# Optimization experiments

Measured on AMD Instinct MI355X. Metric: run time of the kernel, lower is better.

The kernel has to match this reference:

```python
import jax, jax.numpy as jnp
import numpy as np

BF16_MIN = -3.3895313892515355e+38  # torch.finfo(torch.bfloat16).min
B, S, D = 2, 2048, 2048
H, KVH = 32, 8
HD = D // H  # 64


def setup_inputs() -> dict:
    key = jax.random.key(0)
    ks = jax.random.split(key, 7)
    scale = 0.02
    x = jax.random.normal(ks[0], (B, S, D), dtype=jnp.float32)
    # rotary tables as in llama2.c: theta = 10000^{-2i/hd}
    inv_freq = 1.0 / (10000.0 ** (np.arange(0, HD, 2, dtype=np.float32) / HD))
    t = np.arange(S, dtype=np.float32)
    freqs = np.outer(t, inv_freq)  # (S, HD//2)
    freqs_cos = jnp.asarray(np.cos(freqs))
    freqs_sin = jnp.asarray(np.sin(freqs))
    wq = jax.random.normal(ks[1], (H * HD, D), dtype=jnp.float32) * scale
    wk = jax.random.normal(ks[2], (KVH * HD, D), dtype=jnp.float32) * scale
    wv = jax.random.normal(ks[3], (KVH * HD, D), dtype=jnp.float32) * scale
    wo = jax.random.normal(ks[4], (D, H * HD), dtype=jnp.float32) * scale
    attn_mask = jnp.ones((B, S), dtype=jnp.int32)
    return {"x": x, "freqs_cos": freqs_cos, "freqs_sin": freqs_sin,
            "wq": wq, "wk": wk, "wv": wv, "wo": wo, "attn_mask": attn_mask}


def _rope(x, cos, sin):
    # x: (b, s, h, hd) -> split into interleaved real/imag pairs
    b, s, h, hd = x.shape
    xr = x[..., 0::2]
    xi = x[..., 1::2]
    cos = cos[None, :, None, :]  # (1, s, 1, hd//2)
    sin = sin[None, :, None, :]
    out_r = xr * cos - xi * sin
    out_i = xr * sin + xi * cos
    return jnp.stack([out_r, out_i], axis=-1).reshape(b, s, h, hd)


def reference(x, freqs_cos, freqs_sin, wq, wk, wv, wo, attn_mask):
    b, s, d = x.shape
    n_rep = H // KVH
    xq = jnp.einsum('bsd,ed->bse', x, wq).reshape(b, s, H, HD)
    xk = jnp.einsum('bsd,ed->bse', x, wk).reshape(b, s, KVH, HD)
    xv = jnp.einsum('bsd,ed->bse', x, wv).reshape(b, s, KVH, HD)
    xq = _rope(xq, freqs_cos, freqs_sin)
    xk = _rope(xk, freqs_cos, freqs_sin)
    # GQA repeat_kv: (b, s, kvh, hd) -> (b, s, kvh*n_rep, hd)
    xk = jnp.repeat(xk, n_rep, axis=2)
    xv = jnp.repeat(xv, n_rep, axis=2)
    # (b, h, s, hd)
    xq = xq.transpose(0, 2, 1, 3)
    xk = xk.transpose(0, 2, 1, 3)
    xv = xv.transpose(0, 2, 1, 3)
    causal = jnp.triu(jnp.full((s, s), BF16_MIN, dtype=x.dtype), k=1)[None, None]
    pad = jnp.where(attn_mask[:, None, :] == 0, BF16_MIN, 0.0).astype(x.dtype)  # (b,1,s) -> broadcast over query
    combined = causal + pad[:, None, :, :]  # (b,1,s,s)
    scores = jnp.einsum('bhqd,bhkd->bhqk', xq, xk) / np.sqrt(HD).astype(x.dtype)
    scores = jax.nn.softmax(scores + combined, axis=-1)
    out = jnp.einsum('bhqk,bhkd->bhqd', scores, xv)
    out = out.transpose(0, 2, 1, 3).reshape(b, s, H * HD)
    return jnp.einsum('bse,de->bsd', out, wo)
```

## Files before the change

### kernel.cpp

```cpp
#include <hip/hip_runtime.h>

typedef unsigned short u16;
typedef unsigned int u32;
typedef __attribute__((ext_vector_type(8))) short bf16x8;
typedef __attribute__((ext_vector_type(4))) float f32x4;

#define S_LEN 2048
#define QKV_N 3072
#define CEXP 0.18033688011f
#define M32C 5.77078016f

__device__ __forceinline__ u16 f2bf(float f) {
  u32 u = __builtin_bit_cast(u32, f);
  u32 r = (u + 0x7FFFu + ((u >> 16) & 1u)) >> 16;
  return (u16)r;
}
__device__ __forceinline__ float b2f(u16 h) {
  u32 u = ((u32)h) << 16;
  return __builtin_bit_cast(float, u);
}
__device__ __forceinline__ u32 cvtpk(float lo, float hi) {
  u32 r;
  asm("v_cvt_pk_bf16_f32 %0, %1, %2" : "=v"(r) : "v"(lo), "v"(hi));
  return r;
}
__device__ __forceinline__ void gload16(const void* g, void* l) {
  __builtin_amdgcn_global_load_lds(
      (const __attribute__((address_space(1))) u32*)g,
      (__attribute__((address_space(3))) u32*)l, 16, 0, 0);
}

__global__ void cast_all(const float* __restrict__ x, const float* __restrict__ wq,
                         const float* __restrict__ wk, const float* __restrict__ wv,
                         const float* __restrict__ wo, u16* __restrict__ xb,
                         u16* __restrict__ wqkvb, u16* __restrict__ wob) {
  int i = blockIdx.x * 256 + threadIdx.x;
  const float* s;
  u16* d;
  int so, dofs;
  if (i < 2097152) {
    s = x; d = xb; so = i; dofs = i;
  } else if (i < 3145728) {
    s = wq; d = wqkvb; so = i - 2097152; dofs = so;
  } else if (i < 3407872) {
    s = wk; d = wqkvb; so = i - 3145728; dofs = so + 1048576;
  } else if (i < 3670016) {
    s = wv; d = wqkvb; so = i - 3407872; dofs = so + 1310720;
  } else {
    s = wo; d = wob; so = i - 3670016; dofs = so;
  }
  float4 v = ((const float4*)s)[so];
  ((uint2*)d)[dofs] = make_uint2(cvtpk(v.x, v.y), cvtpk(v.z, v.w));
}

template <int BN, int WM, int WN, int OUT_BF16>
__global__ __launch_bounds__(512, 2) void gemm_bt2(const u16* __restrict__ A,
                                                   const u16* __restrict__ B,
                                                   void* __restrict__ Cv,
                                                   int K, int ldc, int nbx) {
  constexpr int BM = 256;
  constexpr int MR = BM / WM / 16;
  constexpr int NR = BN / WN / 16;
  constexpr int MR2 = MR / 2, NR2 = NR / 2;
  constexpr int AR = BM / 64, BR = BN / 64;
  __shared__ u16 As0[BM * 64], As1[BM * 64];
  __shared__ u16 Bs0[BN * 64], Bs1[BN * 64];

  const int tid = threadIdx.x;
  const int lane = tid & 63, w = tid >> 6;
  const int wm = w / WN, wn = w % WN;
  const int g = lane >> 4, r16 = lane & 15;
  const int swz = r16 & 7;

  const int nwg = gridDim.x;
  const int q = nwg >> 3, r = nwg & 7;
  const int xcd = blockIdx.x & 7, off = blockIdx.x >> 3;
  const int wg = (xcd < r ? xcd * (q + 1) : r * (q + 1) + (xcd - r) * q) + off;
  const int m0 = (wg / nbx) * BM, n0 = (wg % nbx) * BN;

  const int rowi = tid >> 3;
  const int scol = ((tid & 7) ^ (rowi & 7)) * 8;
  const u16* Ag0 = A + (size_t)(m0 + rowi) * K + scol;
  const u16* Bg0 = B + (size_t)(n0 + rowi) * K + scol;

  f32x4 acc[MR][NR];
#pragma unroll
  for (int mi = 0; mi < MR; ++mi)
#pragma unroll
    for (int ni = 0; ni < NR; ++ni) acc[mi][ni] = f32x4{0.f, 0.f, 0.f, 0.f};

  auto stage = [&](int kb, u16* Ad, u16* Bd) {
#pragma unroll
    for (int rr = 0; rr < AR; ++rr)
      gload16(Ag0 + (size_t)rr * 64 * K + kb, Ad + rr * 4096 + tid * 8);
#pragma unroll
    for (int rr = 0; rr < BR; ++rr)
      gload16(Bg0 + (size_t)rr * 64 * K + kb, Bd + rr * 4096 + tid * 8);
  };

  auto compute = [&](const u16* Asrc, const u16* Bsrc) {
    bf16x8 ac[MR2][2], bc[NR][2];
    const u16* Aw = Asrc + (wm * MR * 16 + r16) * 64;
    const u16* Bw = Bsrc + (wn * NR * 16 + r16) * 64;
#pragma unroll
    for (int mi = 0; mi < MR2; ++mi)
#pragma unroll
      for (int kk = 0; kk < 2; ++kk)
        ac[mi][kk] = *(const bf16x8*)(Aw + mi * 1024 + ((kk * 4 + g) ^ swz) * 8);
#pragma unroll
    for (int ni = 0; ni < NR2; ++ni)
#pragma unroll
      for (int kk = 0; kk < 2; ++kk)
        bc[ni][kk] = *(const bf16x8*)(Bw + ni * 1024 + ((kk * 4 + g) ^ swz) * 8);
    __builtin_amdgcn_s_setprio(1);
#pragma unroll
    for (int mi = 0; mi < MR2; ++mi)
#pragma unroll
      for (int ni = 0; ni < NR2; ++ni)
#pragma unroll
        for (int kk = 0; kk < 2; ++kk)
          acc[mi][ni] = __builtin_amdgcn_mfma_f32_16x16x32_bf16(
              ac[mi][kk], bc[ni][kk], acc[mi][ni], 0, 0, 0);
    __builtin_amdgcn_s_setprio(0);
#pragma unroll
    for (int ni = NR2; ni < NR; ++ni)
#pragma unroll
      for (int kk = 0; kk < 2; ++kk)
        bc[ni][kk] = *(const bf16x8*)(Bw + ni * 1024 + ((kk * 4 + g) ^ swz) * 8);
    __builtin_amdgcn_s_setprio(1);
#pragma unroll
    for (int mi = 0; mi < MR2; ++mi)
#pragma unroll
      for (int ni = NR2; ni < NR; ++ni)
#pragma unroll
        for (int kk = 0; kk < 2; ++kk)
          acc[mi][ni] = __builtin_amdgcn_mfma_f32_16x16x32_bf16(
              ac[mi][kk], bc[ni][kk], acc[mi][ni], 0, 0, 0);
    __builtin_amdgcn_s_setprio(0);
#pragma unroll
    for (int mi = 0; mi < MR2; ++mi)
#pragma unroll
      for (int kk = 0; kk < 2; ++kk)
        ac[mi][kk] =
            *(const bf16x8*)(Aw + (MR2 + mi) * 1024 + ((kk * 4 + g) ^ swz) * 8);
    __builtin_amdgcn_s_setprio(1);
#pragma unroll
    for (int mi = 0; mi < MR2; ++mi)
#pragma unroll
      for (int ni = NR2; ni < NR; ++ni)
#pragma unroll
        for (int kk = 0; kk < 2; ++kk)
          acc[MR2 + mi][ni] = __builtin_amdgcn_mfma_f32_16x16x32_bf16(
              ac[mi][kk], bc[ni][kk], acc[MR2 + mi][ni], 0, 0, 0);
    __builtin_amdgcn_s_setprio(0);
    __builtin_amdgcn_s_setprio(1);
#pragma unroll
    for (int mi = 0; mi < MR2; ++mi)
#pragma unroll
      for (int ni = 0; ni < NR2; ++ni)
#pragma unroll
        for (int kk = 0; kk < 2; ++kk)
          acc[MR2 + mi][ni] = __builtin_amdgcn_mfma_f32_16x16x32_bf16(
              ac[mi][kk], bc[ni][kk], acc[MR2 + mi][ni], 0, 0, 0);
    __builtin_amdgcn_s_setprio(0);
  };

  const int NT = K >> 6;
  stage(0, As0, Bs0);
  __syncthreads();
  for (int t = 0; t < NT; t += 2) {
    if (t + 1 < NT) stage((t + 1) * 64, As1, Bs1);
    compute(As0, Bs0);
    __syncthreads();
    if (t + 2 < NT) stage((t + 2) * 64, As0, Bs0);
    compute(As1, Bs1);
    __syncthreads();
  }

#pragma unroll
  for (int mi = 0; mi < MR; ++mi)
#pragma unroll
    for (int ni = 0; ni < NR; ++ni) {
      int row = m0 + wm * MR * 16 + mi * 16 + g * 4;
      int col = n0 + wn * NR * 16 + ni * 16 + r16;
#pragma unroll
      for (int j = 0; j < 4; ++j) {
        if (OUT_BF16)
          ((u16*)Cv)[(size_t)(row + j) * ldc + col] = f2bf(acc[mi][ni][j]);
        else
          ((float*)Cv)[(size_t)(row + j) * ldc + col] = acc[mi][ni][j];
      }
    }
}

__global__ void rope_k(u16* qkv, const float* __restrict__ fc,
                       const float* __restrict__ fs) {
  const int p = blockIdx.x * 256 + threadIdx.x;
  const int row = blockIdx.y;
  const int s = row & (S_LEN - 1);
  const int i = p & 31;
  const float c = fc[s * 32 + i], sn = fs[s * 32 + i];
  u32 v = *(const u32*)&qkv[(size_t)row * QKV_N + 2 * p];
  float xr = b2f((u16)(v & 0xffffu)), xi = b2f((u16)(v >> 16));
  float orr = xr * c - xi * sn;
  float oi = xr * sn + xi * c;
  *(u32*)&qkv[(size_t)row * QKV_N + 2 * p] = cvtpk(orr, oi);
}

__global__ void vtrans_k(const u16* __restrict__ qkv, u16* __restrict__ vt) {
  int i = blockIdx.x * 256 + threadIdx.x;
  int s = i & 2047;
  int d = (i >> 11) & 63;
  int bk = i >> 17;
  int b = bk >> 3, kv = bk & 7;
  vt[i] = qkv[(size_t)(b * 2048 + s) * QKV_N + 2560 + kv * 64 + d];
}

__global__ __launch_bounds__(256, 3) void attn_fwd(const u16* __restrict__ qkv,
                                                   const u16* __restrict__ vt,
                                                   u16* __restrict__ aout) {
  __shared__ u16 Ks[2][64 * 64];
  __shared__ u16 Vs[2][64 * 64];
  __shared__ u16 Ps[4][16 * 64];

  const int bh = blockIdx.x;
  const int y = blockIdx.y;
  const int qt = (y < 4) ? (15 - y) : (y < 8) ? (y - 4) : (y < 12) ? y : (19 - y);
  const int b = bh >> 5, h = bh & 31, kvh = h >> 2;
  const int tid = threadIdx.x;
  const int w = tid >> 6, lane = tid & 63;
  const int g = lane >> 4, r16 = lane & 15;
  const int q0w = qt * 128 + w * 32;

  const u16* kbase = qkv + (size_t)b * S_LEN * QKV_N + 2048 + kvh * 64;
  const u16* vbase = vt + (size_t)(b * 8 + kvh) * 64 * S_LEN;

  const int srow = lane >> 3;
  const int scol = ((lane & 7) * 8) ^ (srow * 8);
  const int swz = (r16 & 7) * 8;

  bf16x8 qf[2][2];
#pragma unroll
  for (int qs = 0; qs < 2; ++qs) {
    const u16* qrow =
        qkv + (size_t)(b * S_LEN + q0w + qs * 16 + r16) * QKV_N + h * 64;
#pragma unroll
    for (int dh = 0; dh < 2; ++dh)
      qf[qs][dh] = *(const bf16x8*)(qrow + dh * 32 + g * 8);
  }

  f32x4 oacc[2][4];
#pragma unroll
  for (int qs = 0; qs < 2; ++qs)
#pragma unroll
    for (int dt = 0; dt < 4; ++dt) oacc[qs][dt] = f32x4{0.f, 0.f, 0.f, 0.f};
  float lsum[2] = {0.f, 0.f};

  const int nt = qt * 2 + 2;
  const int ntw = ((q0w + 31) >> 6) + 1;

#pragma unroll
  for (int c2 = 0; c2 < 2; ++c2) {
    int c = w * 2 + c2;
    gload16(kbase + (size_t)(c * 8 + srow) * QKV_N + scol, &Ks[0][c * 512]);
    gload16(vbase + (size_t)(c * 8 + srow) * 2048 + scol, &Vs[0][c * 512]);
  }
  __syncthreads();

  int cur = 0;
  for (int t = 0; t < nt; ++t) {
    if (t + 1 < nt) {
      int kk0 = (t + 1) * 64;
#pragma unroll
      for (int c2 = 0; c2 < 2; ++c2) {
        int c = w * 2 + c2;
        gload16(kbase + (size_t)(kk0 + c * 8 + srow) * QKV_N + scol,
                &Ks[cur ^ 1][c * 512]);
        gload16(vbase + (size_t)(c * 8 + srow) * 2048 + kk0 + scol,
                &Vs[cur ^ 1][c * 512]);
      }
    }
    if (t < ntw) {
      const int k0 = t * 64;
      bf16x8 kf[4][2];
#pragma unroll
      for (int ks = 0; ks < 4; ++ks)
#pragma unroll
        for (int dh = 0; dh < 2; ++dh)
          kf[ks][dh] = *(const bf16x8*)&Ks[cur][(ks * 16 + r16) * 64 +
                                               ((dh * 32 + g * 8) ^ swz)];
      bf16x8 vfc[2][4];
#pragma unroll
      for (int ks2 = 0; ks2 < 2; ++ks2)
#pragma unroll
        for (int dt = 0; dt < 4; ++dt)
          vfc[ks2][dt] = *(const bf16x8*)&Vs[cur][(dt * 16 + r16) * 64 +
                                                  ((ks2 * 32 + g * 8) ^ swz)];
      const bool needmask = (k0 + 63 > q0w);
#pragma unroll
      for (int qs = 0; qs < 2; ++qs) {
        f32x4 st[4];
        __builtin_amdgcn_s_setprio(1);
#pragma unroll
        for (int ks = 0; ks < 4; ++ks) {
          f32x4 a = f32x4{0.f, 0.f, 0.f, 0.f};
          a = __builtin_amdgcn_mfma_f32_16x16x32_bf16(kf[ks][0], qf[qs][0], a, 0, 0, 0);
          a = __builtin_amdgcn_mfma_f32_16x16x32_bf16(kf[ks][1], qf[qs][1], a, 0, 0, 0);
          st[ks] = a;
        }
        __builtin_amdgcn_s_setprio(0);
        const int qg = q0w + qs * 16 + r16;
        if (needmask) {
#pragma unroll
          for (int ks = 0; ks < 4; ++ks)
#pragma unroll
            for (int j = 0; j < 4; ++j)
              if (k0 + ks * 16 + g * 4 + j > qg) st[ks][j] = -__builtin_inff();
        }
        float ps = 0.f;
#pragma unroll
        for (int ks = 0; ks < 4; ++ks) {
          float p0 = exp2f(fmaf(st[ks][0], CEXP, -M32C));
          float p1 = exp2f(fmaf(st[ks][1], CEXP, -M32C));
          float p2 = exp2f(fmaf(st[ks][2], CEXP, -M32C));
          float p3 = exp2f(fmaf(st[ks][3], CEXP, -M32C));
          ps += (p0 + p1) + (p2 + p3);
          *(uint2*)&Ps[w][r16 * 64 + ((ks * 16 + g * 4) ^ swz)] =
              make_uint2(cvtpk(p0, p1), cvtpk(p2, p3));
        }
        lsum[qs] += ps;
        __builtin_amdgcn_s_setprio(1);
#pragma unroll
        for (int ks2 = 0; ks2 < 2; ++ks2) {
          bf16x8 pf =
              *(const bf16x8*)&Ps[w][r16 * 64 + ((ks2 * 32 + g * 8) ^ swz)];
#pragma unroll
          for (int dt = 0; dt < 4; ++dt)
            oacc[qs][dt] = __builtin_amdgcn_mfma_f32_16x16x32_bf16(
                pf, vfc[ks2][dt], oacc[qs][dt], 0, 0, 0);
        }
        __builtin_amdgcn_s_setprio(0);
      }
    }
    __syncthreads();
    cur ^= 1;
  }

#pragma unroll
  for (int qs = 0; qs < 2; ++qs) {
    float l = lsum[qs];
    l += __shfl_xor(l, 16);
    l += __shfl_xor(l, 32);
    float inv = 1.f / l;
    float iv[4];
#pragma unroll
    for (int j = 0; j < 4; ++j) iv[j] = __shfl(inv, g * 4 + j);
#pragma unroll
    for (int dt = 0; dt < 4; ++dt)
#pragma unroll
      for (int j = 0; j < 4; ++j) {
        size_t o = (size_t)(b * S_LEN + q0w + qs * 16 + g * 4 + j) * 2048 +
                   h * 64 + dt * 16 + r16;
        aout[o] = f2bf(oacc[qs][dt][j] * iv[j]);
      }
  }
}

extern "C" void kernel_launch(void* const* d_in, const int* in_sizes, int n_in,
                              void* d_out, int out_size, void* d_ws,
                              size_t ws_size, hipStream_t stream) {
  const float* x = (const float*)d_in[0];
  const float* fc = (const float*)d_in[1];
  const float* fs = (const float*)d_in[2];
  const float* wq = (const float*)d_in[3];
  const float* wk = (const float*)d_in[4];
  const float* wv = (const float*)d_in[5];
  const float* wo = (const float*)d_in[6];
  float* out = (float*)d_out;

  char* ws = (char*)d_ws;
  u16* xb = (u16*)(ws);
  u16* wqkvb = (u16*)(ws + 16777216);
  u16* wob = (u16*)(ws + 29360128);
  u16* qkvb = (u16*)(ws + 37748736);
  u16* vtb = (u16*)(ws + 62914560);
  u16* aoutb = (u16*)(ws + 67108864);

  cast_all<<<18432, 256, 0, stream>>>(x, wq, wk, wv, wo, xb, wqkvb, wob);

  gemm_bt2<256, 2, 4, 1><<<192, 512, 0, stream>>>(xb, wqkvb, qkvb, 2048, 3072, 12);
  rope_k<<<dim3(5, 4096), 256, 0, stream>>>(qkvb, fc, fs);
  vtrans_k<<<8192, 256, 0, stream>>>(qkvb, vtb);
  attn_fwd<<<dim3(64, 16), 256, 0, stream>>>(qkvb, vtb, aoutb);
  gemm_bt2<128, 4, 2, 0><<<256, 512, 0, stream>>>(aoutb, wob, out, 2048, 2048, 16);
}
```

Baseline: 191.4 us.

## Fuse RoPE into QKV GEMM epilogue and single-buffer attention K/V tiles

Removes the separate rope kernel: the QKV GEMM epilogue rotates Q and K columns in fp32 before the bf16 store, fetching the paired element with a lane shuffle. This saves a full read-modify-write pass over the Q/K buffer and one launch, and also skips an intermediate bf16 rounding. Separately, attention K/V LDS tiles become single-buffered: fragments are loaded into registers, then after a barrier the next tile's async load is issued so it overlaps compute. This halves the LDS footprint, which may allow more resident blocks, at the cost of an extra barrier per iteration.

After: 275.6 us. 44.0% more time.

```diff
diff --git a/kernel.cpp b/kernel.cpp
--- a/kernel.cpp
+++ b/kernel.cpp
@@ -14,10 +14,6 @@
   u32 u = __builtin_bit_cast(u32, f);
   u32 r = (u + 0x7FFFu + ((u >> 16) & 1u)) >> 16;
   return (u16)r;
-}
-__device__ __forceinline__ float b2f(u16 h) {
-  u32 u = ((u32)h) << 16;
-  return __builtin_bit_cast(float, u);
 }
 __device__ __forceinline__ u32 cvtpk(float lo, float hi) {
   u32 r;
@@ -53,11 +49,13 @@
   ((uint2*)d)[dofs] = make_uint2(cvtpk(v.x, v.y), cvtpk(v.z, v.w));
 }
 
-template <int BN, int WM, int WN, int OUT_BF16>
+template <int BN, int WM, int WN, int OUT_BF16, int ROPE>
 __global__ __launch_bounds__(512, 2) void gemm_bt2(const u16* __restrict__ A,
                                                    const u16* __restrict__ B,
                                                    void* __restrict__ Cv,
-                                                   int K, int ldc, int nbx) {
+                                                   int K, int ldc, int nbx,
+                                                   const float* __restrict__ fc,
+                                                   const float* __restrict__ fs) {
   constexpr int BM = 256;
   constexpr int MR = BM / WM / 16;
   constexpr int NR = BN / WN / 16;
@@ -185,26 +183,22 @@
       int col = n0 + wn * NR * 16 + ni * 16 + r16;
 #pragma unroll
       for (int j = 0; j < 4; ++j) {
+        float v = acc[mi][ni][j];
+        if (ROPE) {
+          float pv = __shfl_xor(v, 1);
+          if (col < 2560) {
+            int s = (row + j) & (S_LEN - 1);
+            int fi = (col >> 1) & 31;
+            float c = fc[s * 32 + fi], sn = fs[s * 32 + fi];
+            v = fmaf(pv, (r16 & 1) ? sn : -sn, v * c);
+          }
+        }
         if (OUT_BF16)
-          ((u16*)Cv)[(size_t)(row + j) * ldc + col] = f2bf(acc[mi][ni][j]);
+          ((u16*)Cv)[(size_t)(row + j) * ldc + col] = f2bf(v);
         else
-          ((float*)Cv)[(size_t)(row + j) * ldc + col] = acc[mi][ni][j];
+          ((float*)Cv)[(size_t)(row + j) * ldc + col] = v;
       }
     }
-}
-
-__global__ void rope_k(u16* qkv, const float* __restrict__ fc,
-                       const float* __restrict__ fs) {
-  const int p = blockIdx.x * 256 + threadIdx.x;
-  const int row = blockIdx.y;
-  const int s = row & (S_LEN - 1);
-  const int i = p & 31;
-  const float c = fc[s * 32 + i], sn = fs[s * 32 + i];
-  u32 v = *(const u32*)&qkv[(size_t)row * QKV_N + 2 * p];
-  float xr = b2f((u16)(v & 0xffffu)), xi = b2f((u16)(v >> 16));
-  float orr = xr * c - xi * sn;
-  float oi = xr * sn + xi * c;
-  *(u32*)&qkv[(size_t)row * QKV_N + 2 * p] = cvtpk(orr, oi);
 }
 
 __global__ void vtrans_k(const u16* __restrict__ qkv, u16* __restrict__ vt) {
@@ -219,8 +213,8 @@
 __global__ __launch_bounds__(256, 3) void attn_fwd(const u16* __restrict__ qkv,
                                                    const u16* __restrict__ vt,
                                                    u16* __restrict__ aout) {
-  __shared__ u16 Ks[2][64 * 64];
-  __shared__ u16 Vs[2][64 * 64];
+  __shared__ u16 Ks[64 * 64];
+  __shared__ u16 Vs[64 * 64];
   __shared__ u16 Ps[4][16 * 64];
 
   const int bh = blockIdx.x;
@@ -262,40 +256,42 @@
 #pragma unroll
   for (int c2 = 0; c2 < 2; ++c2) {
     int c = w * 2 + c2;
-    gload16(kbase + (size_t)(c * 8 + srow) * QKV_N + scol, &Ks[0][c * 512]);
-    gload16(vbase + (size_t)(c * 8 + srow) * 2048 + scol, &Vs[0][c * 512]);
-  }
-  __syncthreads();
-
-  int cur = 0;
+    gload16(kbase + (size_t)(c * 8 + srow) * QKV_N + scol, &Ks[c * 512]);
+    gload16(vbase + (size_t)(c * 8 + srow) * 2048 + scol, &Vs[c * 512]);
+  }
+
   for (int t = 0; t < nt; ++t) {
+    __syncthreads();
+    bf16x8 kf[4][2];
+    bf16x8 vfc[2][4];
+    if (t < ntw) {
+#pragma unroll
+      for (int ks = 0; ks < 4; ++ks)
+#pragma unroll
+        for (int dh = 0; dh < 2; ++dh)
+          kf[ks][dh] = *(const bf16x8*)&Ks[(ks * 16 + r16) * 64 +
+                                          ((dh * 32 + g * 8) ^ swz)];
+#pragma unroll
+      for (int ks2 = 0; ks2 < 2; ++ks2)
+#pragma unroll
+        for (int dt = 0; dt < 4; ++dt)
+          vfc[ks2][dt] = *(const bf16x8*)&Vs[(dt * 16 + r16) * 64 +
+                                             ((ks2 * 32 + g * 8) ^ swz)];
+    }
+    __syncthreads();
     if (t + 1 < nt) {
       int kk0 = (t + 1) * 64;
 #pragma unroll
       for (int c2 = 0; c2 < 2; ++c2) {
         int c = w * 2 + c2;
         gload16(kbase + (size_t)(kk0 + c * 8 + srow) * QKV_N + scol,
-                &Ks[cur ^ 1][c * 512]);
+                &Ks[c * 512]);
         gload16(vbase + (size_t)(c * 8 + srow) * 2048 + kk0 + scol,
-                &Vs[cur ^ 1][c * 512]);
+                &Vs[c * 512]);
       }
     }
     if (t < ntw) {
       const int k0 = t * 64;
-      bf16x8 kf[4][2];
-#pragma unroll
-      for (int ks = 0; ks < 4; ++ks)
-#pragma unroll
-        for (int dh = 0; dh < 2; ++dh)
-          kf[ks][dh] = *(const bf16x8*)&Ks[cur][(ks * 16 + r16) * 64 +
-                                               ((dh * 32 + g * 8) ^ swz)];
-      bf16x8 vfc[2][4];
-#pragma unroll
-      for (int ks2 = 0; ks2 < 2; ++ks2)
-#pragma unroll
-        for (int dt = 0; dt < 4; ++dt)
-          vfc[ks2][dt] = *(const bf16x8*)&Vs[cur][(dt * 16 + r16) * 64 +
-                                                  ((ks2 * 32 + g * 8) ^ swz)];
       const bool needmask = (k0 + 63 > q0w);
 #pragma unroll
       for (int qs = 0; qs < 2; ++qs) {
@@ -342,8 +338,6 @@
         __builtin_amdgcn_s_setprio(0);
       }
     }
-    __syncthreads();
-    cur ^= 1;
   }
 
 #pragma unroll
@@ -388,9 +382,10 @@
 
   cast_all<<<18432, 256, 0, stream>>>(x, wq, wk, wv, wo, xb, wqkvb, wob);
 
-  gemm_bt2<256, 2, 4, 1><<<192, 512, 0, stream>>>(xb, wqkvb, qkvb, 2048, 3072, 12);
-  rope_k<<<dim3(5, 4096), 256, 0, stream>>>(qkvb, fc, fs);
+  gemm_bt2<256, 2, 4, 1, 1><<<192, 512, 0, stream>>>(xb, wqkvb, qkvb, 2048,
+                                                     3072, 12, fc, fs);
   vtrans_k<<<8192, 256, 0, stream>>>(qkvb, vtb);
   attn_fwd<<<dim3(64, 16), 256, 0, stream>>>(qkvb, vtb, aoutb);
-  gemm_bt2<128, 4, 2, 0><<<256, 512, 0, stream>>>(aoutb, wob, out, 2048, 2048, 16);
-}
+  gemm_bt2<128, 4, 2, 0, 0><<<256, 512, 0, stream>>>(aoutb, wob, out, 2048,
+                                                     2048, 16, nullptr, nullptr);
+}
```
